# Optimization experiments

Hardware: AMD Instinct MI355X
Metric: run time of the kernel (lower is better)

The kernel has to match this reference:

```python
import jax, jax.numpy as jnp
import numpy as np

N_NODES = 20000
N_EDGES = 320000
IN_F = 256
OUT_F = 64
HEADS = 4
ALPHA = 0.1  # leaky_relu negative slope


def setup_inputs() -> dict:
    key = jax.random.key(0)
    ks = jax.random.split(key, 8)
    return {
        "input1": jax.random.normal(ks[0], (N_NODES, IN_F), jnp.float32),
        "input2": jax.random.normal(ks[1], (N_NODES, IN_F), jnp.float32),
        # per-head params: Ws maps source feats -> target_out, Wt maps target feats -> source_out
        "Ws": jax.random.normal(ks[2], (HEADS, IN_F, OUT_F), jnp.float32) * 0.06,
        "Wt": jax.random.normal(ks[3], (HEADS, IN_F, OUT_F), jnp.float32) * 0.06,
        "a1": jax.random.normal(ks[4], (HEADS, 2 * OUT_F), jnp.float32) * 0.1,
        "a2": jax.random.normal(ks[5], (HEADS, 2 * OUT_F), jnp.float32) * 0.1,
        # COO nonzeros of A_opt [n_target, n_source]
        "tgt_idx": jax.random.randint(ks[6], (N_EDGES,), 0, N_NODES),
        "src_idx": jax.random.randint(ks[7], (N_EDGES,), 0, N_NODES),
    }


def _segment_softmax(scores, seg, num_segments):
    m = jax.lax.stop_gradient(jax.ops.segment_max(scores, seg, num_segments=num_segments))
    w = jnp.exp(scores - m[seg])
    d = jax.ops.segment_sum(w, seg, num_segments=num_segments)
    d = jnp.where(d == 0, 1.0, d)
    return w / d[seg]


def _head(x1, x2, Ws, Wt, a1, a2, src, tgt, n_s, n_t):
    s = x1 @ Ws  # [n_s, OUT_F]  messages source -> target
    t = x2 @ Wt  # [n_t, OUT_F]  messages target -> source
    out = Ws.shape[1]
    # edge score e = leaky_relu(a^T [s_src || t_tgt]); split a to avoid edge-level concat
    e1 = jax.nn.leaky_relu((s @ a1[:out])[src] + (t @ a1[out:])[tgt], ALPHA)
    e2 = jax.nn.leaky_relu((s @ a2[:out])[src] + (t @ a2[out:])[tgt], ALPHA)
    alpha_ts = _segment_softmax(e1, tgt, n_t)  # softmax over sources per target
    alpha_st = _segment_softmax(e2, src, n_s)  # softmax over targets per source
    h_ts = jax.ops.segment_sum(alpha_ts[:, None] * s[src], tgt, num_segments=n_t)
    h_st = jax.ops.segment_sum(alpha_st[:, None] * t[tgt], src, num_segments=n_s)
    return jax.nn.elu(h_st), jax.nn.elu(h_ts)  # concat=True -> ELU per head


def reference(input1, input2, Ws, Wt, a1, a2, tgt_idx, src_idx):
    n_s, n_t = input1.shape[0], input2.shape[0]
    head_fn = jax.vmap(
        lambda W1, W2, v1, v2: _head(input1, input2, W1, W2, v1, v2, src_idx, tgt_idx, n_s, n_t)
    )
    h_st, h_ts = head_fn(Ws, Wt, a1, a2)  # each [H, n, OUT_F]
    h_st = jnp.transpose(h_st, (1, 0, 2)).reshape(n_s, -1)  # concat heads
    h_ts = jnp.transpose(h_ts, (1, 0, 2)).reshape(n_t, -1)
    return h_st, h_ts
```

## Files before the change

kernel.cpp:

```cpp
#include <hip/hip_runtime.h>
#include <math.h>

#define N_NODES 20000
#define N_EDGES 320000
#define IN_F 256
#define OUT_F 64
#define HEADS 4
#define NCOL 256
#define LRELU_ALPHA 0.1f
#define ELL_CAP 64

#define SCAT_X 313
#define GEMM_GB 157
#define CST_STRIDE 136

typedef __attribute__((ext_vector_type(8))) short short8;
typedef __attribute__((ext_vector_type(4))) float floatx4;

__device__ __forceinline__ float lrelu(float x) {
    return x > 0.f ? x : LRELU_ALPHA * x;
}
__device__ __forceinline__ unsigned short f2bf(float f) {
    unsigned int u = __float_as_uint(f);
    u = (u + 0x7FFF + ((u >> 16) & 1)) >> 16;
    return (unsigned short)u;
}
__device__ __forceinline__ float bf2f(unsigned short u) {
    return __uint_as_float(((unsigned int)u) << 16);
}

__global__ __launch_bounds__(256) void prep_w_kernel(
    const float* __restrict__ Ws, const float* __restrict__ Wt,
    unsigned short* __restrict__ Wsb, unsigned short* __restrict__ Wtb,
    int* __restrict__ cnt)
{
    const int gid = blockIdx.x * 256 + threadIdx.x;

    for (int i = gid; i < 2 * N_NODES; i += 16384) cnt[i] = 0;

    const int mat = gid >> 13;
    const int r   = gid & 8191;
    const int kc  = r >> 8;
    const int c   = r & 255;
    const float* W    = mat ? Wt : Ws;
    unsigned short* O = mat ? Wtb : Wsb;
    const int h = c >> 6, j = c & 63;
    const int k0 = kc * 8;
    unsigned short v[8] __attribute__((aligned(16)));
#pragma unroll
    for (int i = 0; i < 8; ++i)
        v[i] = f2bf(W[(size_t)h * (IN_F * OUT_F) + (size_t)(k0 + i) * OUT_F + j]);
    *(uint4*)(O + (size_t)c * IN_F + k0) = *(const uint4*)v;
}

__global__ __launch_bounds__(512, 4) void hybrid_kernel(
    const float* __restrict__ A0, const unsigned short* __restrict__ Wb0,
    const float* __restrict__ A1, const unsigned short* __restrict__ Wb1,
    unsigned short* __restrict__ C0, unsigned short* __restrict__ C1,
    const float* __restrict__ a1, const float* __restrict__ a2,
    float* __restrict__ ss1, float* __restrict__ ss2,
    float* __restrict__ tt1, float* __restrict__ tt2,
    const int* __restrict__ src, const int* __restrict__ tgt,
    int* __restrict__ cnt_t, int* __restrict__ cnt_s,
    unsigned short* __restrict__ elist_t, unsigned short* __restrict__ elist_s)
{
    const int tid = threadIdx.x;

    __shared__ __align__(16) unsigned short Bl[128][264];

    if (blockIdx.x < SCAT_X) {
        const int e = ((int)blockIdx.y * SCAT_X + (int)blockIdx.x) * 512 + tid;
        if (e < N_EDGES) {
            const int s = src[e], t = tgt[e];
            const int p = atomicAdd(&cnt_t[t], 1);
            const int q = atomicAdd(&cnt_s[s], 1);
            if (p < ELL_CAP) elist_t[t * ELL_CAP + p] = (unsigned short)s;
            if (q < ELL_CAP) elist_s[s * ELL_CAP + q] = (unsigned short)t;
        }
        return;
    }

    const int gx   = blockIdx.x - SCAT_X;
    const int half = gx & 1;
    const int gb   = gx >> 1;
    const float* A           = (blockIdx.y == 0) ? A0 : A1;
    const unsigned short* Wb = (blockIdx.y == 0) ? Wb0 : Wb1;
    unsigned short* C        = (blockIdx.y == 0) ? C0 : C1;

    for (int i = tid; i < 4096; i += 512) {
        const int n  = i >> 5;
        const int kc = (i & 31) << 3;
        *(uint4*)&Bl[n][kc] = *(const uint4*)(Wb + (size_t)(half * 128 + n) * IN_F + kc);
    }
    __syncthreads();

    const int lane = tid & 63;
    const int w    = tid >> 6;
    const int quad = lane >> 4;
    const int l15  = lane & 15;
    const int g    = gb * 8 + w;
    const bool live = (g < 1250);

    floatx4 acc[8];
#pragma unroll
    for (int c = 0; c < 8; ++c) acc[c] = (floatx4){0.f, 0.f, 0.f, 0.f};

    if (live) {
        const float* arow = A + (size_t)(g * 16 + l15) * IN_F + quad * 8;

        float4 ua[8];
#pragma unroll
        for (int kk = 0; kk < 4; ++kk) {
            ua[2 * kk]     = *(const float4*)(arow + kk * 32);
            ua[2 * kk + 1] = *(const float4*)(arow + kk * 32 + 4);
        }
        short8 af[4];
#pragma unroll
        for (int kk = 0; kk < 4; ++kk) {
            short8 t;
            t[0] = (short)f2bf(ua[2 * kk].x);     t[1] = (short)f2bf(ua[2 * kk].y);
            t[2] = (short)f2bf(ua[2 * kk].z);     t[3] = (short)f2bf(ua[2 * kk].w);
            t[4] = (short)f2bf(ua[2 * kk + 1].x); t[5] = (short)f2bf(ua[2 * kk + 1].y);
            t[6] = (short)f2bf(ua[2 * kk + 1].z); t[7] = (short)f2bf(ua[2 * kk + 1].w);
            af[kk] = t;
        }

        float4 ub[8];
#pragma unroll
        for (int kk = 0; kk < 4; ++kk) {
            ub[2 * kk]     = *(const float4*)(arow + (kk + 4) * 32);
            ub[2 * kk + 1] = *(const float4*)(arow + (kk + 4) * 32 + 4);
        }

#pragma unroll
        for (int kk = 0; kk < 4; ++kk) {
#pragma unroll
            for (int c = 0; c < 8; ++c) {
                short8 bfrag = *(const short8*)&Bl[c * 16 + l15][kk * 32 + quad * 8];
                acc[c] = __builtin_amdgcn_mfma_f32_16x16x32_bf16(af[kk], bfrag, acc[c], 0, 0, 0);
            }
        }

#pragma unroll
        for (int kk = 0; kk < 4; ++kk) {
            short8 t;
            t[0] = (short)f2bf(ub[2 * kk].x);     t[1] = (short)f2bf(ub[2 * kk].y);
            t[2] = (short)f2bf(ub[2 * kk].z);     t[3] = (short)f2bf(ub[2 * kk].w);
            t[4] = (short)f2bf(ub[2 * kk + 1].x); t[5] = (short)f2bf(ub[2 * kk + 1].y);
            t[6] = (short)f2bf(ub[2 * kk + 1].z); t[7] = (short)f2bf(ub[2 * kk + 1].w);
            af[kk] = t;
        }
#pragma unroll
        for (int kk = 0; kk < 4; ++kk) {
#pragma unroll
            for (int c = 0; c < 8; ++c) {
                short8 bfrag = *(const short8*)&Bl[c * 16 + l15][(kk + 4) * 32 + quad * 8];
                acc[c] = __builtin_amdgcn_mfma_f32_16x16x32_bf16(af[kk], bfrag, acc[c], 0, 0, 0);
            }
        }

        const int off_aj = (blockIdx.y == 0) ? 0 : 64;
        float* o1 = (blockIdx.y == 0) ? ss1 : tt1;
        float* o2 = (blockIdx.y == 0) ? ss2 : tt2;

        float p1[2][4] = {{0.f,0.f,0.f,0.f},{0.f,0.f,0.f,0.f}};
        float p2[2][4] = {{0.f,0.f,0.f,0.f},{0.f,0.f,0.f,0.f}};
#pragma unroll
        for (int c = 0; c < 8; ++c) {
            const int hl = c >> 2;
            const int hh = half * 2 + hl;
            const int jj = (c & 3) * 16 + l15;
            const float w1 = a1[hh * 128 + off_aj + jj];
            const float w2 = a2[hh * 128 + off_aj + jj];
#pragma unroll
            for (int r = 0; r < 4; ++r) {
                p1[hl][r] += acc[c][r] * w1;
                p2[hl][r] += acc[c][r] * w2;
            }
        }
#pragma unroll
        for (int m = 1; m < 16; m <<= 1) {
#pragma unroll
            for (int hl = 0; hl < 2; ++hl)
#pragma unroll
                for (int r = 0; r < 4; ++r) {
                    p1[hl][r] += __shfl_xor(p1[hl][r], m, 64);
                    p2[hl][r] += __shfl_xor(p2[hl][r], m, 64);
                }
        }
        if (l15 == 0) {
#pragma unroll
            for (int r = 0; r < 4; ++r) {
                const int m = g * 16 + quad * 4 + r;
#pragma unroll
                for (int hl = 0; hl < 2; ++hl) {
                    const int hh = half * 2 + hl;
                    o1[m * HEADS + hh] = p1[hl][r];
                    o2[m * HEADS + hh] = p2[hl][r];
                }
            }
        }
    }

    __syncthreads();
    unsigned short* Cst = &Bl[0][0];

    if (live) {
#pragma unroll
        for (int c = 0; c < 8; ++c) {
            const int lc = c * 16 + l15;
#pragma unroll
            for (int r = 0; r < 4; ++r) {
                const int lr = w * 16 + quad * 4 + r;
                Cst[lr * CST_STRIDE + lc] = f2bf(acc[c][r]);
            }
        }
    }
    __syncthreads();

    {
        const int cx = tid & 15;
        const int rbase = tid >> 4;
#pragma unroll
        for (int it = 0; it < 4; ++it) {
            const int lr = it * 32 + rbase;
            const int mrow = gb * 128 + lr;
            if (mrow < N_NODES) {
                uint4 v = *(const uint4*)&Cst[lr * CST_STRIDE + cx * 8];
                *(uint4*)(C + (size_t)mrow * NCOL + half * 128 + cx * 8) = v;
            }
        }
    }
}

__global__ __launch_bounds__(256) void agg_kernel(
    const int* __restrict__ cnt_t, const unsigned short* __restrict__ elist_t,
    const int* __restrict__ cnt_s, const unsigned short* __restrict__ elist_s,
    const float* __restrict__ ss1, const float* __restrict__ ss2,
    const float* __restrict__ tt1, const float* __restrict__ tt2,
    const unsigned short* __restrict__ s_bf, const unsigned short* __restrict__ t_bf,
    float* __restrict__ h_st, float* __restrict__ h_ts)
{
    const int b    = blockIdx.x;
    const int dir  = b & 1;
    const int wave = threadIdx.x >> 6;
    const int lane = threadIdx.x & 63;
    const int n    = (b >> 1) * 4 + wave;
    const int h    = lane >> 4;
    const int coff = lane * 4;

    const int*            cnt   = dir ? cnt_s   : cnt_t;
    const unsigned short* list  = dir ? elist_s : elist_t;
    const unsigned short* table = dir ? t_bf    : s_bf;
    const float*          nsc   = dir ? ss2     : tt1;
    const float*          esc   = dir ? tt2     : ss1;
    float*                outp  = dir ? h_st    : h_ts;

    const float base = nsc[n * HEADS + h];
    int deg = cnt[n];
    if (deg > ELL_CAP) deg = ELL_CAP;
    const int b0 = n * ELL_CAP, b1 = b0 + deg;

    float4 acc = make_float4(0.f, 0.f, 0.f, 0.f);
    float den = 0.f;

    int p = b0;
    for (; p + 3 < b1; p += 4) {
        int m0 = list[p],     m1 = list[p + 1];
        int m2 = list[p + 2], m3 = list[p + 3];
        float e0 = esc[m0 * HEADS + h], e1 = esc[m1 * HEADS + h];
        float e2 = esc[m2 * HEADS + h], e3 = esc[m3 * HEADS + h];
        ushort4 r0 = *(const ushort4*)(table + (size_t)m0 * NCOL + coff);
        ushort4 r1 = *(const ushort4*)(table + (size_t)m1 * NCOL + coff);
        ushort4 r2 = *(const ushort4*)(table + (size_t)m2 * NCOL + coff);
        ushort4 r3 = *(const ushort4*)(table + (size_t)m3 * NCOL + coff);
        float w0 = __expf(lrelu(e0 + base));
        float w1 = __expf(lrelu(e1 + base));
        float w2 = __expf(lrelu(e2 + base));
        float w3 = __expf(lrelu(e3 + base));
        den += (w0 + w1) + (w2 + w3);
        acc.x += (w0 * bf2f(r0.x) + w1 * bf2f(r1.x)) + (w2 * bf2f(r2.x) + w3 * bf2f(r3.x));
        acc.y += (w0 * bf2f(r0.y) + w1 * bf2f(r1.y)) + (w2 * bf2f(r2.y) + w3 * bf2f(r3.y));
        acc.z += (w0 * bf2f(r0.z) + w1 * bf2f(r1.z)) + (w2 * bf2f(r2.z) + w3 * bf2f(r3.z));
        acc.w += (w0 * bf2f(r0.w) + w1 * bf2f(r1.w)) + (w2 * bf2f(r2.w) + w3 * bf2f(r3.w));
    }
    for (; p < b1; ++p) {
        int m0 = list[p];
        float w0 = __expf(lrelu(esc[m0 * HEADS + h] + base));
        ushort4 r0 = *(const ushort4*)(table + (size_t)m0 * NCOL + coff);
        den += w0;
        acc.x += w0 * bf2f(r0.x);
        acc.y += w0 * bf2f(r0.y);
        acc.z += w0 * bf2f(r0.z);
        acc.w += w0 * bf2f(r0.w);
    }

    if (den == 0.f) den = 1.f;
    float inv = 1.f / den;
    float4 r;
    r.x = acc.x * inv; r.y = acc.y * inv; r.z = acc.z * inv; r.w = acc.w * inv;
    r.x = (r.x > 0.f) ? r.x : expm1f(r.x);
    r.y = (r.y > 0.f) ? r.y : expm1f(r.y);
    r.z = (r.z > 0.f) ? r.z : expm1f(r.z);
    r.w = (r.w > 0.f) ? r.w : expm1f(r.w);
    *(float4*)(outp + (size_t)n * NCOL + coff) = r;
}

extern "C" void kernel_launch(void* const* d_in, const int* in_sizes, int n_in,
                              void* d_out, int out_size, void* d_ws, size_t ws_size,
                              hipStream_t stream)
{
    const float* input1 = (const float*)d_in[0];
    const float* input2 = (const float*)d_in[1];
    const float* Ws     = (const float*)d_in[2];
    const float* Wt     = (const float*)d_in[3];
    const float* a1     = (const float*)d_in[4];
    const float* a2     = (const float*)d_in[5];
    const int*   tgt    = (const int*)d_in[6];
    const int*   src    = (const int*)d_in[7];

    float* out  = (float*)d_out;
    float* h_st = out;
    float* h_ts = out + (size_t)N_NODES * NCOL;

    unsigned short* s_bf = (unsigned short*)d_ws;
    unsigned short* t_bf = s_bf + (size_t)N_NODES * NCOL;
    unsigned short* Wsb  = t_bf + (size_t)N_NODES * NCOL;
    unsigned short* Wtb  = Wsb + 256 * 256;
    float* ss1  = (float*)(Wtb + 256 * 256);
    float* ss2  = ss1 + N_NODES * HEADS;
    float* tt1  = ss2 + N_NODES * HEADS;
    float* tt2  = tt1 + N_NODES * HEADS;
    int*   cnt_t = (int*)(tt2 + N_NODES * HEADS);
    int*   cnt_s = cnt_t + N_NODES;
    unsigned short* elist_t = (unsigned short*)(cnt_s + N_NODES);
    unsigned short* elist_s = elist_t + (size_t)N_NODES * ELL_CAP;

    prep_w_kernel<<<64, 256, 0, stream>>>(Ws, Wt, Wsb, Wtb, cnt_t);

    dim3 ggrid(SCAT_X + GEMM_GB * 2, 2);
    hybrid_kernel<<<ggrid, 512, 0, stream>>>(input1, Wsb, input2, Wtb,
                                             s_bf, t_bf, a1, a2,
                                             ss1, ss2, tt1, tt2,
                                             src, tgt, cnt_t, cnt_s,
                                             elist_t, elist_s);

    agg_kernel<<<10000, 256, 0, stream>>>(cnt_t, elist_t, cnt_s, elist_s,
                                          ss1, ss2, tt1, tt2, s_bf, t_bf, h_st, h_ts);
}
```

Before: 181.7 us.

## Split aggregation per head and parallelize edge softmax across lanes

Each wave now processes one (node, head) pair instead of one node across all heads. Edge weights are computed in parallel across lanes, reduced with shuffles, and staged in shared memory. Four edges are then gathered concurrently by 16-lane groups and combined with a cross-group shuffle reduction. The aim is to cut serial per-edge latency and raise memory parallelism. The cost is four times more blocks, redundant count and list reads, and a possible out-of-bounds shared read for degrees near the cap.

```diff
diff --git a/kernel.cpp b/kernel.cpp
--- a/kernel.cpp
+++ b/kernel.cpp
@@ -13,6 +13,7 @@
 #define SCAT_X 313
 #define GEMM_GB 157
 #define CST_STRIDE 136
+#define AGG_BLOCKS 40000
 
 typedef __attribute__((ext_vector_type(8))) short short8;
 typedef __attribute__((ext_vector_type(4))) float floatx4;
@@ -241,13 +242,13 @@
     const unsigned short* __restrict__ s_bf, const unsigned short* __restrict__ t_bf,
     float* __restrict__ h_st, float* __restrict__ h_ts)
 {
-    const int b    = blockIdx.x;
-    const int dir  = b & 1;
-    const int wave = threadIdx.x >> 6;
-    const int lane = threadIdx.x & 63;
-    const int n    = (b >> 1) * 4 + wave;
-    const int h    = lane >> 4;
-    const int coff = lane * 4;
+    const int b     = blockIdx.x;
+    const int slice = b & 7;
+    const int dir   = slice >> 2;
+    const int h     = slice & 3;
+    const int wv    = threadIdx.x >> 6;
+    const int lane  = threadIdx.x & 63;
+    const int n     = (b >> 3) * 4 + wv;
 
     const int*            cnt   = dir ? cnt_s   : cnt_t;
     const unsigned short* list  = dir ? elist_s : elist_t;
@@ -256,54 +257,66 @@
     const float*          esc   = dir ? tt2     : ss1;
     float*                outp  = dir ? h_st    : h_ts;
 
-    const float base = nsc[n * HEADS + h];
+    __shared__ uint2 wm[4][64];
+    uint2* wmrow = wm[wv];
+
     int deg = cnt[n];
     if (deg > ELL_CAP) deg = ELL_CAP;
-    const int b0 = n * ELL_CAP, b1 = b0 + deg;
+
+    const int  mraw = list[n * ELL_CAP + lane];
+    const bool act  = lane < deg;
+    const int  m    = act ? mraw : 0;
+    const float ev   = esc[m * HEADS + h];
+    const float base = nsc[n * HEADS + h];
+    float w = act ? __expf(lrelu(ev + base)) : 0.f;
+
+    float den = w;
+#pragma unroll
+    for (int msk = 1; msk < 64; msk <<= 1) den += __shfl_xor(den, msk, 64);
+    const float inv = (den == 0.f) ? 1.f : 1.f / den;
+
+    wmrow[lane] = make_uint2(__float_as_uint(w),
+                             (unsigned)(m * (NCOL * 2) + h * 128));
+
+    __syncthreads();
+
+    const int el   = lane >> 4;
+    const int l15  = lane & 15;
+    const unsigned cbyte = (unsigned)(l15 * 8);
+    const char* tb = (const char*)table;
 
     float4 acc = make_float4(0.f, 0.f, 0.f, 0.f);
-    float den = 0.f;
-
-    int p = b0;
-    for (; p + 3 < b1; p += 4) {
-        int m0 = list[p],     m1 = list[p + 1];
-        int m2 = list[p + 2], m3 = list[p + 3];
-        float e0 = esc[m0 * HEADS + h], e1 = esc[m1 * HEADS + h];
-        float e2 = esc[m2 * HEADS + h], e3 = esc[m3 * HEADS + h];
-        ushort4 r0 = *(const ushort4*)(table + (size_t)m0 * NCOL + coff);
-        ushort4 r1 = *(const ushort4*)(table + (size_t)m1 * NCOL + coff);
-        ushort4 r2 = *(const ushort4*)(table + (size_t)m2 * NCOL + coff);
-        ushort4 r3 = *(const ushort4*)(table + (size_t)m3 * NCOL + coff);
-        float w0 = __expf(lrelu(e0 + base));
-        float w1 = __expf(lrelu(e1 + base));
-        float w2 = __expf(lrelu(e2 + base));
-        float w3 = __expf(lrelu(e3 + base));
-        den += (w0 + w1) + (w2 + w3);
-        acc.x += (w0 * bf2f(r0.x) + w1 * bf2f(r1.x)) + (w2 * bf2f(r2.x) + w3 * bf2f(r3.x));
-        acc.y += (w0 * bf2f(r0.y) + w1 * bf2f(r1.y)) + (w2 * bf2f(r2.y) + w3 * bf2f(r3.y));
-        acc.z += (w0 * bf2f(r0.z) + w1 * bf2f(r1.z)) + (w2 * bf2f(r2.z) + w3 * bf2f(r3.z));
-        acc.w += (w0 * bf2f(r0.w) + w1 * bf2f(r1.w)) + (w2 * bf2f(r2.w) + w3 * bf2f(r3.w));
-    }
-    for (; p < b1; ++p) {
-        int m0 = list[p];
-        float w0 = __expf(lrelu(esc[m0 * HEADS + h] + base));
-        ushort4 r0 = *(const ushort4*)(table + (size_t)m0 * NCOL + coff);
-        den += w0;
-        acc.x += w0 * bf2f(r0.x);
-        acc.y += w0 * bf2f(r0.y);
-        acc.z += w0 * bf2f(r0.z);
-        acc.w += w0 * bf2f(r0.w);
-    }
-
-    if (den == 0.f) den = 1.f;
-    float inv = 1.f / den;
-    float4 r;
-    r.x = acc.x * inv; r.y = acc.y * inv; r.z = acc.z * inv; r.w = acc.w * inv;
-    r.x = (r.x > 0.f) ? r.x : expm1f(r.x);
-    r.y = (r.y > 0.f) ? r.y : expm1f(r.y);
-    r.z = (r.z > 0.f) ? r.z : expm1f(r.z);
-    r.w = (r.w > 0.f) ? r.w : expm1f(r.w);
-    *(float4*)(outp + (size_t)n * NCOL + coff) = r;
+    for (int p = 0; p < deg; p += 8) {
+        uint2 a0 = wmrow[p + el];
+        uint2 a1 = wmrow[p + 4 + el];
+        float w0 = __uint_as_float(a0.x);
+        float w1 = __uint_as_float(a1.x);
+        ushort4 r0 = *(const ushort4*)(tb + (a0.y + cbyte));
+        ushort4 r1 = *(const ushort4*)(tb + (a1.y + cbyte));
+        acc.x += w0 * bf2f(r0.x) + w1 * bf2f(r1.x);
+        acc.y += w0 * bf2f(r0.y) + w1 * bf2f(r1.y);
+        acc.z += w0 * bf2f(r0.z) + w1 * bf2f(r1.z);
+        acc.w += w0 * bf2f(r0.w) + w1 * bf2f(r1.w);
+    }
+
+#pragma unroll
+    for (int msk = 16; msk < 64; msk <<= 1) {
+        acc.x += __shfl_xor(acc.x, msk, 64);
+        acc.y += __shfl_xor(acc.y, msk, 64);
+        acc.z += __shfl_xor(acc.z, msk, 64);
+        acc.w += __shfl_xor(acc.w, msk, 64);
+    }
+
+    if (el == 0) {
+        float4 r;
+        r.x = acc.x * inv; r.y = acc.y * inv;
+        r.z = acc.z * inv; r.w = acc.w * inv;
+        r.x = (r.x > 0.f) ? r.x : expm1f(r.x);
+        r.y = (r.y > 0.f) ? r.y : expm1f(r.y);
+        r.z = (r.z > 0.f) ? r.z : expm1f(r.z);
+        r.w = (r.w > 0.f) ? r.w : expm1f(r.w);
+        *(float4*)(outp + (size_t)n * NCOL + h * 64 + l15 * 4) = r;
+    }
 }
 
 extern "C" void kernel_launch(void* const* d_in, const int* in_sizes, int n_in,
@@ -345,6 +358,7 @@
                                              src, tgt, cnt_t, cnt_s,
                                              elist_t, elist_s);
 
-    agg_kernel<<<10000, 256, 0, stream>>>(cnt_t, elist_t, cnt_s, elist_s,
-                                          ss1, ss2, tt1, tt2, s_bf, t_bf, h_st, h_ts);
-}
+    agg_kernel<<<AGG_BLOCKS, 256, 0, stream>>>(cnt_t, elist_t, cnt_s, elist_s,
+                                               ss1, ss2, tt1, tt2, s_bf, t_bf,
+                                               h_st, h_ts);
+}
```

Result: slower. 201.6 us (+11.0%).
